# Optimization experiments

Hardware: AMD Instinct MI355X
Metric: run time of the kernel (lower is better)

## Reference

```python
import jax, jax.numpy as jnp
import numpy as np

B, S1, S2, S3, I, O = 4, 64, 64, 64, 32, 32
MX, MZ = 16, 16
HID = O * 2  # factor=2 feedforward hidden


def setup_inputs() -> dict:
    key = jax.random.key(0)
    ks = jax.random.split(key, 5)
    x = jax.random.normal(ks[0], (B, S1, S2, S3, I), jnp.float32)
    # xavier-normal-ish scale for complex fourier weights stored as [...,2]
    sw = np.float32(np.sqrt(2.0 / (I + O)))
    wx = jax.random.normal(ks[1], (I, O, MX, 2), jnp.float32) * sw
    wz = jax.random.normal(ks[2], (I, O, MZ, 2), jnp.float32) * sw
    w1 = jax.random.normal(ks[3], (O, HID), jnp.float32) * np.float32(np.sqrt(1.0 / O))
    b1 = jnp.zeros((HID,), jnp.float32)
    w2 = jax.random.normal(ks[4], (HID, O), jnp.float32) * np.float32(np.sqrt(1.0 / HID))
    b2 = jnp.zeros((O,), jnp.float32)
    return {"x": x, "wx": wx, "wz": wz, "w1": w1, "b1": b1, "w2": w2, "b2": b2}


def _forward_fourier(x, wx, wz):
    # x: [b, i, s1, s2, s3]
    # z-axis branch
    cwz = wz[..., 0] + 1j * wz[..., 1]          # [i, o, mz] complex
    xfz = jnp.fft.rfft(x, axis=-1, norm='ortho')  # [b,i,s1,s2,S3//2+1]
    pz = jnp.einsum('bixyz,ioz->boxyz', xfz[..., :MZ], cwz)
    pz = jnp.pad(pz, ((0, 0), (0, 0), (0, 0), (0, 0), (0, S3 // 2 + 1 - MZ)))
    xz = jnp.fft.irfft(pz, n=S3, axis=-1, norm='ortho')
    # x-axis branch (note: modes_y branch contributes 0 in the source, xy=0.0)
    cwx = wx[..., 0] + 1j * wx[..., 1]          # [i, o, mx]
    xfx = jnp.fft.rfft(x, axis=2, norm='ortho')  # [b,i,S1//2+1,s2,s3]
    px = jnp.einsum('bixyz,iox->boxyz', xfx[:, :, :MX], cwx)
    px = jnp.pad(px, ((0, 0), (0, 0), (0, S1 // 2 + 1 - MX), (0, 0), (0, 0)))
    xx = jnp.fft.irfft(px, n=S1, axis=2, norm='ortho')
    return xx + xz


def reference(x, wx, wz, w1, b1, w2, b2):
    xt = jnp.transpose(x, (0, 4, 1, 2, 3))      # b i s1 s2 s3
    y = _forward_fourier(xt, wx, wz)
    y = jnp.transpose(y, (0, 2, 3, 4, 1))       # b s1 s2 s3 o
    # backcast FeedForward: Linear -> ReLU -> Linear (dropout=0, no norms)
    h = jax.nn.relu(y @ w1 + b1)
    b_out = h @ w2 + b2
    return b_out
```

## Files before the change

### kernel.cpp

```cpp
#include <hip/hip_runtime.h>

namespace {

typedef _Float16 half_t;
typedef half_t f16x8 __attribute__((ext_vector_type(8)));
typedef float f32x4 __attribute__((ext_vector_type(4)));

constexpr size_t RSTR = 64 * 64 * 32;

constexpr int WS_TF = 0;
constexpr int WS_TI = 2048;
constexpr int WS_WZ = 4096;
constexpr int WS_WX = 69632;
constexpr int WS_W1 = 135168;
constexpr int WS_W2 = 137216;

__device__ __forceinline__ float f4get(const float4& v, int u) {
  return u == 0 ? v.x : (u == 1 ? v.y : (u == 2 ? v.z : v.w));
}

__device__ __forceinline__ f32x4 mfma16(f16x8 a, f16x8 b, f32x4 c) {
  return __builtin_amdgcn_mfma_f32_16x16x32_f16(a, b, c, 0, 0, 0);
}

__global__ __launch_bounds__(256) void kinit(const float* __restrict__ wx,
                                             const float* __restrict__ wz,
                                             const float* __restrict__ w1,
                                             const float* __restrict__ w2,
                                             half_t* __restrict__ wsh) {
  const int id = blockIdx.x * 256 + threadIdx.x;
  const int l = id & 63, r = l & 15, g = l >> 4;
  f16x8 frag;
  if (id < 256) {
    int fid = id >> 6, mt = fid >> 1, kt = fid & 1;
#pragma unroll
    for (int e = 0; e < 8; ++e) {
      int k = kt * 32 + 8 * g + e;
      int mc = mt * 16 + r, m = mc >> 1, p = mc & 1;
      float s, c;
      sincospif((float)(m * k) * (1.0f / 32.0f), &s, &c);
      frag[e] = (half_t)(0.125f * (p ? -s : c));
    }
    *(f16x8*)(wsh + WS_TF + (size_t)id * 8) = frag;
  } else if (id < 512) {
    int id2 = id - 256, mt = id2 >> 6;
#pragma unroll
    for (int e = 0; e < 8; ++e) {
      int zp = mt * 16 + r;
      int k = 8 * g + e, m = k >> 1, p = k & 1;
      float s, c;
      sincospif((float)(m * zp) * (1.0f / 32.0f), &s, &c);
      float sc = (m == 0) ? 0.125f : 0.25f;
      frag[e] = (half_t)(p ? -sc * s : sc * c);
    }
    *(f16x8*)(wsh + WS_TI + (size_t)id2 * 8) = frag;
  } else if (id < 16896) {
    int id2 = id - 512;
    const float* wsrc = wz;
    size_t off = WS_WZ;
    if (id2 >= 8192) { id2 -= 8192; wsrc = wx; off = WS_WX; }
    int fid = id2 >> 6, m = fid >> 3, kt = (fid >> 2) & 1, nt = fid & 3;
#pragma unroll
    for (int e = 0; e < 8; ++e) {
      int k = kt * 32 + 8 * g + e, i = k >> 1, p = k & 1;
      int n = nt * 16 + r, o = n >> 1, q = n & 1;
      int base = ((i * 32 + o) * 16 + m) * 2;
      float re = wsrc[base], im = wsrc[base + 1];
      frag[e] = (half_t)(q ? (p ? re : im) : (p ? -im : re));
    }
    *(f16x8*)(wsh + off + (size_t)id2 * 8) = frag;
  } else if (id < 17152) {
    int id2 = id - 16896, nt = id2 >> 6;
#pragma unroll
    for (int e = 0; e < 8; ++e) {
      int k = 8 * g + e, n = nt * 16 + r;
      frag[e] = (half_t)w1[k * 64 + n];
    }
    *(f16x8*)(wsh + WS_W1 + (size_t)id2 * 8) = frag;
  } else if (id < 17408) {
    int id2 = id - 17152, fid = id2 >> 6, kt = fid >> 1, nt = fid & 1;
#pragma unroll
    for (int e = 0; e < 8; ++e) {
      int k = kt * 32 + 8 * g + e, n = nt * 16 + r;
      frag[e] = (half_t)w2[k * 32 + n];
    }
    *(f16x8*)(wsh + WS_W2 + (size_t)id2 * 8) = frag;
  }
}

template <int BR>
__global__ __launch_bounds__(256) void kspec(const float* __restrict__ x,
                                             const half_t* __restrict__ wsh,
                                             const float* __restrict__ b1g,
                                             const float* __restrict__ b2g,
                                             float* __restrict__ outf) {
  __shared__ __align__(16) char smraw[49152];
  half_t* XB = (half_t*)smraw;
  half_t* FB = (half_t*)smraw;
  half_t* PB = (half_t*)(smraw + 32768);
  half_t* YL = (half_t*)smraw;
  half_t* HL = (half_t*)(smraw + 32768);
  half_t* outh = (half_t*)outf;
  const int t = threadIdx.x, l = t & 63, w = t >> 6, r = l & 15, g = l >> 4;
  const f32x4 vzero = {0.f, 0.f, 0.f, 0.f};

  const int col0 = blockIdx.x * 8;
  int b = 0, s2 = 0, s30 = 0;
  size_t xbase, zstr, cstr;
  if (BR == 0) {
    xbase = (size_t)col0 * 2048; zstr = 32; cstr = 2048;
  } else {
    b = col0 >> 12; s2 = (col0 >> 6) & 63; s30 = col0 & 63;
    xbase = (size_t)b * 8388608 + (size_t)s2 * 2048 + (size_t)s30 * 32;
    zstr = RSTR; cstr = 32;
  }

  {
    int c = t >> 5, sub = t & 31;
    int i4 = (sub & 7) * 4, zq = sub >> 3;
    const float* xp = x + xbase + (size_t)c * cstr + i4;
#pragma unroll
    for (int zo = 0; zo < 2; ++zo) {
      int zb = zq * 16 + zo * 8;
      float4 v[8];
#pragma unroll
      for (int zz = 0; zz < 8; ++zz)
        v[zz] = *(const float4*)(xp + (size_t)(zb + zz) * zstr);
#pragma unroll
      for (int u = 0; u < 4; ++u) {
        f16x8 rowv;
#pragma unroll
        for (int zz = 0; zz < 8; ++zz) rowv[zz] = (half_t)f4get(v[zz], u);
        int rowi = c * 32 + i4 + u;
        int gr = (zb >> 3) ^ (rowi & 7);
        *(f16x8*)(XB + rowi * 64 + gr * 8) = rowv;
      }
    }
  }
  __syncthreads();

  f32x4 fa[2][4];
#pragma unroll
  for (int mt = 0; mt < 2; ++mt)
#pragma unroll
    for (int nt = 0; nt < 4; ++nt) fa[mt][nt] = vzero;
  {
    f16x8 Atf[2][2], Bx[4][2];
#pragma unroll
    for (int mt = 0; mt < 2; ++mt)
#pragma unroll
      for (int kt = 0; kt < 2; ++kt)
        Atf[mt][kt] = *(const f16x8*)(wsh + WS_TF + (size_t)((mt * 2 + kt) * 64 + l) * 8);
#pragma unroll
    for (int nt = 0; nt < 4; ++nt)
#pragma unroll
      for (int kt = 0; kt < 2; ++kt) {
        int rowi = w * 64 + nt * 16 + r;
        int gr = (kt * 4 + g) ^ (rowi & 7);
        Bx[nt][kt] = *(const f16x8*)(XB + rowi * 64 + gr * 8);
      }
#pragma unroll
    for (int kt = 0; kt < 2; ++kt)
#pragma unroll
      for (int nt = 0; nt < 4; ++nt)
#pragma unroll
        for (int mt = 0; mt < 2; ++mt)
          fa[mt][nt] = mfma16(Atf[mt][kt], Bx[nt][kt], fa[mt][nt]);
  }
  __syncthreads();

#pragma unroll
  for (int mt = 0; mt < 2; ++mt)
#pragma unroll
    for (int nt = 0; nt < 4; ++nt)
#pragma unroll
      for (int q = 0; q < 4; ++q) {
        int mc = mt * 16 + 4 * g + q, m = mc >> 1, p = mc & 1;
        int n = w * 64 + nt * 16 + r, c = n >> 5, i = n & 31;
        int k = 2 * i + p;
        FB[(m * 16 + c) * 64 + ((k >> 3) ^ (c & 7)) * 8 + (k & 7)] = (half_t)fa[mt][nt][q];
      }
  __syncthreads();

  const half_t* WF = wsh + (BR == 0 ? WS_WZ : WS_WX);
#pragma unroll
  for (int j = 0; j < 4; ++j) {
    int m = w * 4 + j;
    f16x8 Af[2];
#pragma unroll
    for (int kt = 0; kt < 2; ++kt) {
      int gr = (kt * 4 + g) ^ (r & 7);
      Af[kt] = *(const f16x8*)(FB + (m * 16 + r) * 64 + gr * 8);
    }
    f32x4 pa[4];
#pragma unroll
    for (int nt = 0; nt < 4; ++nt) pa[nt] = vzero;
#pragma unroll
    for (int kt = 0; kt < 2; ++kt)
#pragma unroll
      for (int nt = 0; nt < 4; ++nt) {
        f16x8 Bw = *(const f16x8*)(WF + (size_t)((m * 8 + kt * 4 + nt) * 64 + l) * 8);
        pa[nt] = mfma16(Af[kt], Bw, pa[nt]);
      }
#pragma unroll
    for (int nt = 0; nt < 4; ++nt)
#pragma unroll
      for (int q = 0; q < 4; ++q) {
        int c = 4 * g + q;
        if (c < 8) {
          int n = nt * 16 + r, o = n >> 1, q2 = n & 1;
          int k = 2 * m + q2;
          PB[(c * 32 + o) * 32 + ((k >> 3) ^ (o & 3)) * 8 + (k & 7)] = (half_t)pa[nt][q];
        }
      }
  }
  __syncthreads();

  {
    f16x8 Ati[4];
#pragma unroll
    for (int mt = 0; mt < 4; ++mt)
      Ati[mt] = *(const f16x8*)(wsh + WS_TI + (size_t)(mt * 64 + l) * 8);
#pragma unroll
    for (int cc = 0; cc < 2; ++cc) {
      int c = w * 2 + cc;
      f16x8 Bp[2];
#pragma unroll
      for (int nt = 0; nt < 2; ++nt) {
        int o = nt * 16 + r;
        Bp[nt] = *(const f16x8*)(PB + (c * 32 + o) * 32 + (g ^ (o & 3)) * 8);
      }
      f32x4 ya[4][2];
#pragma unroll
      for (int mt = 0; mt < 4; ++mt)
#pragma unroll
        for (int nt = 0; nt < 2; ++nt) ya[mt][nt] = mfma16(Ati[mt], Bp[nt], vzero);
#pragma unroll
      for (int mt = 0; mt < 4; ++mt)
#pragma unroll
        for (int nt = 0; nt < 2; ++nt)
#pragma unroll
          for (int q = 0; q < 4; ++q) {
            int zp = mt * 16 + 4 * g + q, o = nt * 16 + r;
            if (BR == 0) {
              outh[(size_t)(col0 + c) * 4096 + zp * 64 + o] = (half_t)ya[mt][nt][q];
            } else {
              size_t kzcol = (size_t)(b * 64 + zp) * 64 + s2;
              float yz = (float)outh[kzcol * 4096 + (s30 + c) * 64 + o];
              float yv = ya[mt][nt][q] + yz;
              int rowi = c * 64 + zp;
              YL[rowi * 32 + ((o >> 3) ^ (rowi & 3)) * 8 + (o & 7)] = (half_t)yv;
            }
          }
    }
  }
  if (BR == 0) return;
  __syncthreads();

  {
    f16x8 W1F[4], W2F[4];
#pragma unroll
    for (int nt = 0; nt < 4; ++nt)
      W1F[nt] = *(const f16x8*)(wsh + WS_W1 + (size_t)(nt * 64 + l) * 8);
#pragma unroll
    for (int f = 0; f < 4; ++f)
      W2F[f] = *(const f16x8*)(wsh + WS_W2 + (size_t)(f * 64 + l) * 8);
    float b1v[4], b2v[2];
#pragma unroll
    for (int nt = 0; nt < 4; ++nt) b1v[nt] = b1g[nt * 16 + r];
#pragma unroll
    for (int nt = 0; nt < 2; ++nt) b2v[nt] = b2g[nt * 16 + r];

    for (int rr = 0; rr < 4; ++rr) {
      f16x8 AY[2];
#pragma unroll
      for (int mt = 0; mt < 2; ++mt) {
        int rowi = rr * 128 + w * 32 + mt * 16 + r;
        AY[mt] = *(const f16x8*)(YL + rowi * 32 + (g ^ (rowi & 3)) * 8);
      }
      f32x4 ha[2][4];
#pragma unroll
      for (int mt = 0; mt < 2; ++mt)
#pragma unroll
        for (int nt = 0; nt < 4; ++nt) ha[mt][nt] = mfma16(AY[mt], W1F[nt], vzero);
#pragma unroll
      for (int mt = 0; mt < 2; ++mt)
#pragma unroll
        for (int nt = 0; nt < 4; ++nt)
#pragma unroll
          for (int q = 0; q < 4; ++q) {
            int rloc = w * 32 + mt * 16 + 4 * g + q, n = nt * 16 + r;
            float hv = fmaxf(ha[mt][nt][q] + b1v[nt], 0.f);
            HL[rloc * 64 + ((n >> 3) ^ (rloc & 7)) * 8 + (n & 7)] = (half_t)hv;
          }
      __syncthreads();
      f16x8 AH[2][2];
#pragma unroll
      for (int mt = 0; mt < 2; ++mt)
#pragma unroll
        for (int kt = 0; kt < 2; ++kt) {
          int rloc = w * 32 + mt * 16 + r;
          AH[mt][kt] = *(const f16x8*)(HL + rloc * 64 + ((kt * 4 + g) ^ (rloc & 7)) * 8);
        }
      f32x4 oa[2][2];
#pragma unroll
      for (int mt = 0; mt < 2; ++mt)
#pragma unroll
        for (int nt = 0; nt < 2; ++nt) oa[mt][nt] = vzero;
#pragma unroll
      for (int kt = 0; kt < 2; ++kt)
#pragma unroll
        for (int mt = 0; mt < 2; ++mt)
#pragma unroll
          for (int nt = 0; nt < 2; ++nt)
            oa[mt][nt] = mfma16(AH[mt][kt], W2F[kt * 2 + nt], oa[mt][nt]);
#pragma unroll
      for (int mt = 0; mt < 2; ++mt)
#pragma unroll
        for (int nt = 0; nt < 2; ++nt)
#pragma unroll
          for (int q = 0; q < 4; ++q) {
            int rowg = rr * 128 + w * 32 + mt * 16 + 4 * g + q;
            int c = rowg >> 6, zp = rowg & 63, o = nt * 16 + r;
            outf[(size_t)b * 8388608 + (size_t)zp * RSTR + (size_t)s2 * 2048 +
                 (size_t)(s30 + c) * 32 + o] = oa[mt][nt][q] + b2v[nt];
          }
      __syncthreads();
    }
  }
}

}

extern "C" void kernel_launch(void* const* d_in, const int* in_sizes, int n_in,
                              void* d_out, int out_size, void* d_ws, size_t ws_size,
                              hipStream_t stream) {
  const float* x = (const float*)d_in[0];
  const float* wx = (const float*)d_in[1];
  const float* wz = (const float*)d_in[2];
  const float* w1 = (const float*)d_in[3];
  const float* b1 = (const float*)d_in[4];
  const float* w2 = (const float*)d_in[5];
  const float* b2 = (const float*)d_in[6];
  float* out = (float*)d_out;
  half_t* wsh = (half_t*)d_ws;

  hipLaunchKernelGGL(kinit, dim3(68), dim3(256), 0, stream, wx, wz, w1, w2, wsh);
  hipLaunchKernelGGL((kspec<0>), dim3(2048), dim3(256), 0, stream, x, wsh, b1, b2, out);
  hipLaunchKernelGGL((kspec<1>), dim3(2048), dim3(256), 0, stream, x, wsh, b1, b2, out);
}
```

Before: 146.1 us.

## Split x-branch into dedicated smaller-tile kernel with reduced LDS and block swizzle

The x-axis branch plus feedforward moves out of the templated kernel into a new kernel that handles 4 columns per block instead of 8. It uses 32KB of shared memory instead of 48KB and asks for 5 blocks per SM, so more blocks can be resident at once. Block indices are remapped so neighbouring blocks spread across s2/b. The z-branch intermediates are prefetched into registers before the inverse-transform MFMA. The cost is twice as many blocks, each reloading the same weight fragments, and possible register pressure from the launch-bounds hint.

```diff
diff --git a/kernel.cpp b/kernel.cpp
--- a/kernel.cpp
+++ b/kernel.cpp
@@ -98,22 +98,12 @@
   half_t* XB = (half_t*)smraw;
   half_t* FB = (half_t*)smraw;
   half_t* PB = (half_t*)(smraw + 32768);
-  half_t* YL = (half_t*)smraw;
-  half_t* HL = (half_t*)(smraw + 32768);
   half_t* outh = (half_t*)outf;
   const int t = threadIdx.x, l = t & 63, w = t >> 6, r = l & 15, g = l >> 4;
   const f32x4 vzero = {0.f, 0.f, 0.f, 0.f};
 
   const int col0 = blockIdx.x * 8;
-  int b = 0, s2 = 0, s30 = 0;
-  size_t xbase, zstr, cstr;
-  if (BR == 0) {
-    xbase = (size_t)col0 * 2048; zstr = 32; cstr = 2048;
-  } else {
-    b = col0 >> 12; s2 = (col0 >> 6) & 63; s30 = col0 & 63;
-    xbase = (size_t)b * 8388608 + (size_t)s2 * 2048 + (size_t)s30 * 32;
-    zstr = RSTR; cstr = 32;
-  }
+  size_t xbase = (size_t)col0 * 2048, zstr = 32, cstr = 2048;
 
   {
     int c = t >> 5, sub = t & 31;
@@ -182,7 +172,7 @@
       }
   __syncthreads();
 
-  const half_t* WF = wsh + (BR == 0 ? WS_WZ : WS_WX);
+  const half_t* WF = wsh + WS_WZ;
 #pragma unroll
   for (int j = 0; j < 4; ++j) {
     int m = w * 4 + j;
@@ -242,19 +232,163 @@
 #pragma unroll
           for (int q = 0; q < 4; ++q) {
             int zp = mt * 16 + 4 * g + q, o = nt * 16 + r;
-            if (BR == 0) {
-              outh[(size_t)(col0 + c) * 4096 + zp * 64 + o] = (half_t)ya[mt][nt][q];
-            } else {
-              size_t kzcol = (size_t)(b * 64 + zp) * 64 + s2;
-              float yz = (float)outh[kzcol * 4096 + (s30 + c) * 64 + o];
-              float yv = ya[mt][nt][q] + yz;
-              int rowi = c * 64 + zp;
-              YL[rowi * 32 + ((o >> 3) ^ (rowi & 3)) * 8 + (o & 7)] = (half_t)yv;
-            }
+            outh[(size_t)(col0 + c) * 4096 + zp * 64 + o] = (half_t)ya[mt][nt][q];
           }
     }
   }
-  if (BR == 0) return;
+}
+
+__global__ __launch_bounds__(256, 5) void kx4(const float* __restrict__ x,
+                                              const half_t* __restrict__ wsh,
+                                              const float* __restrict__ b1g,
+                                              const float* __restrict__ b2g,
+                                              float* __restrict__ outf) {
+  __shared__ __align__(16) half_t smh[16384];
+  half_t* XB = smh;
+  half_t* FB = smh + 8192;
+  half_t* PB = smh + 12288;
+  half_t* YL = smh;
+  half_t* HL = smh + 8192;
+  half_t* outh = (half_t*)outf;
+  const int t = threadIdx.x, l = t & 63, w = t >> 6, r = l & 15, g = l >> 4;
+  const f32x4 vzero = {0.f, 0.f, 0.f, 0.f};
+
+  const int d = blockIdx.x;
+  const int p = (d & 7) * 512 + (d >> 3);
+  const int col0 = p * 4;
+  const int b = col0 >> 12, s2 = (col0 >> 6) & 63, s30 = col0 & 63;
+  const size_t xbase = (size_t)b * 8388608 + (size_t)s2 * 2048 + (size_t)s30 * 32;
+
+  {
+    int sub = t & 31, zq = t >> 5;
+    int c = sub >> 3, i4 = (sub & 7) * 4;
+    const float* xp = x + xbase + (size_t)c * 32 + i4 + (size_t)(zq * 8) * RSTR;
+    float4 v[8];
+#pragma unroll
+    for (int zz = 0; zz < 8; ++zz) v[zz] = *(const float4*)(xp + (size_t)zz * RSTR);
+#pragma unroll
+    for (int uu = 0; uu < 4; ++uu) {
+      int u = (uu + sub) & 3;
+      f16x8 rowv;
+#pragma unroll
+      for (int zz = 0; zz < 8; ++zz) rowv[zz] = (half_t)f4get(v[zz], u);
+      int rowi = c * 32 + i4 + u;
+      *(f16x8*)(XB + rowi * 64 + (zq ^ (rowi & 7)) * 8) = rowv;
+    }
+  }
+  __syncthreads();
+
+  f32x4 fa[2][2];
+  {
+    f16x8 Atf[2][2], Bx[2][2];
+#pragma unroll
+    for (int mt = 0; mt < 2; ++mt)
+#pragma unroll
+      for (int kt = 0; kt < 2; ++kt)
+        Atf[mt][kt] = *(const f16x8*)(wsh + WS_TF + (size_t)((mt * 2 + kt) * 64 + l) * 8);
+#pragma unroll
+    for (int nt = 0; nt < 2; ++nt)
+#pragma unroll
+      for (int kt = 0; kt < 2; ++kt) {
+        int rowi = w * 32 + nt * 16 + r;
+        Bx[nt][kt] = *(const f16x8*)(XB + rowi * 64 + (((kt * 4 + g) ^ (rowi & 7))) * 8);
+      }
+#pragma unroll
+    for (int mt = 0; mt < 2; ++mt)
+#pragma unroll
+      for (int nt = 0; nt < 2; ++nt) fa[mt][nt] = vzero;
+#pragma unroll
+    for (int kt = 0; kt < 2; ++kt)
+#pragma unroll
+      for (int nt = 0; nt < 2; ++nt)
+#pragma unroll
+        for (int mt = 0; mt < 2; ++mt)
+          fa[mt][nt] = mfma16(Atf[mt][kt], Bx[nt][kt], fa[mt][nt]);
+  }
+#pragma unroll
+  for (int mt = 0; mt < 2; ++mt)
+#pragma unroll
+    for (int nt = 0; nt < 2; ++nt)
+#pragma unroll
+      for (int q = 0; q < 4; ++q) {
+        int mc = mt * 16 + 4 * g + q, m = mc >> 1, pp = mc & 1;
+        int n = w * 32 + nt * 16 + r, c = n >> 5, i = n & 31;
+        int k = 2 * i + pp;
+        FB[(m * 4 + c) * 64 + (((k >> 3) ^ ((m + 2 * c) & 7))) * 8 + (k & 7)] =
+            (half_t)fa[mt][nt][q];
+      }
+  __syncthreads();
+
+#pragma unroll
+  for (int j = 0; j < 4; ++j) {
+    int m = w * 4 + j;
+    int rsel = r & 3, keym = (m + 2 * rsel) & 7;
+    f16x8 Af[2];
+#pragma unroll
+    for (int kt = 0; kt < 2; ++kt)
+      Af[kt] = *(const f16x8*)(FB + (m * 4 + rsel) * 64 + (((kt * 4 + g) ^ keym)) * 8);
+    f32x4 pa[4];
+#pragma unroll
+    for (int nt = 0; nt < 4; ++nt) pa[nt] = vzero;
+#pragma unroll
+    for (int kt = 0; kt < 2; ++kt)
+#pragma unroll
+      for (int nt = 0; nt < 4; ++nt) {
+        f16x8 Bw = *(const f16x8*)(wsh + WS_WX + (size_t)((m * 8 + kt * 4 + nt) * 64 + l) * 8);
+        pa[nt] = mfma16(Af[kt], Bw, pa[nt]);
+      }
+    if (g == 0) {
+#pragma unroll
+      for (int nt = 0; nt < 4; ++nt)
+#pragma unroll
+        for (int q = 0; q < 4; ++q) {
+          int c = q;
+          int n = nt * 16 + r, o = n >> 1, q2 = n & 1;
+          int k = 2 * m + q2;
+          PB[(c * 32 + o) * 32 + (((k >> 3) ^ (o & 3))) * 8 + (k & 7)] = (half_t)pa[nt][q];
+        }
+    }
+  }
+  __syncthreads();
+
+  {
+    half_t yzr[4][2][4];
+    const half_t* yzp = outh + ((size_t)b * 4096 + s2) * 4096 + (size_t)(s30 + w) * 64 +
+                        (size_t)(4 * g) * 262144 + r;
+#pragma unroll
+    for (int mt = 0; mt < 4; ++mt)
+#pragma unroll
+      for (int q = 0; q < 4; ++q)
+#pragma unroll
+        for (int nt = 0; nt < 2; ++nt)
+          yzr[mt][nt][q] = yzp[(size_t)(mt * 16 + q) * 262144 + nt * 16];
+
+    f16x8 Ati[4], Bp[2];
+#pragma unroll
+    for (int mt = 0; mt < 4; ++mt)
+      Ati[mt] = *(const f16x8*)(wsh + WS_TI + (size_t)(mt * 64 + l) * 8);
+#pragma unroll
+    for (int nt = 0; nt < 2; ++nt) {
+      int o = nt * 16 + r;
+      Bp[nt] = *(const f16x8*)(PB + (w * 32 + o) * 32 + ((g ^ (o & 3))) * 8);
+    }
+    f32x4 ya[4][2];
+#pragma unroll
+    for (int mt = 0; mt < 4; ++mt)
+#pragma unroll
+      for (int nt = 0; nt < 2; ++nt) ya[mt][nt] = mfma16(Ati[mt], Bp[nt], vzero);
+#pragma unroll
+    for (int mt = 0; mt < 4; ++mt)
+#pragma unroll
+      for (int nt = 0; nt < 2; ++nt)
+#pragma unroll
+        for (int q = 0; q < 4; ++q) {
+          int zp = mt * 16 + 4 * g + q, o = nt * 16 + r;
+          float acc = ya[mt][nt][q] + (float)yzr[mt][nt][q];
+          int rowi = w * 64 + zp;
+          YL[rowi * 32 + (((o >> 3) ^ ((rowi >> 2) & 3))) * 8 + (o & 7)] = (half_t)acc;
+        }
+  }
   __syncthreads();
 
   {
@@ -272,60 +406,41 @@
     for (int nt = 0; nt < 2; ++nt) b2v[nt] = b2g[nt * 16 + r];
 
     for (int rr = 0; rr < 4; ++rr) {
-      f16x8 AY[2];
-#pragma unroll
-      for (int mt = 0; mt < 2; ++mt) {
-        int rowi = rr * 128 + w * 32 + mt * 16 + r;
-        AY[mt] = *(const f16x8*)(YL + rowi * 32 + (g ^ (rowi & 3)) * 8);
-      }
-      f32x4 ha[2][4];
-#pragma unroll
-      for (int mt = 0; mt < 2; ++mt)
-#pragma unroll
-        for (int nt = 0; nt < 4; ++nt) ha[mt][nt] = mfma16(AY[mt], W1F[nt], vzero);
-#pragma unroll
-      for (int mt = 0; mt < 2; ++mt)
-#pragma unroll
-        for (int nt = 0; nt < 4; ++nt)
-#pragma unroll
-          for (int q = 0; q < 4; ++q) {
-            int rloc = w * 32 + mt * 16 + 4 * g + q, n = nt * 16 + r;
-            float hv = fmaxf(ha[mt][nt][q] + b1v[nt], 0.f);
-            HL[rloc * 64 + ((n >> 3) ^ (rloc & 7)) * 8 + (n & 7)] = (half_t)hv;
-          }
+      int rowA = rr * 64 + w * 16 + r;
+      f16x8 AY = *(const f16x8*)(YL + rowA * 32 + ((g ^ ((rowA >> 2) & 3))) * 8);
+      f32x4 ha[4];
+#pragma unroll
+      for (int nt = 0; nt < 4; ++nt) ha[nt] = mfma16(AY, W1F[nt], vzero);
+#pragma unroll
+      for (int nt = 0; nt < 4; ++nt)
+#pragma unroll
+        for (int q = 0; q < 4; ++q) {
+          int rloc = w * 16 + 4 * g + q, n = nt * 16 + r;
+          float hv = fmaxf(ha[nt][q] + b1v[nt], 0.f);
+          HL[rloc * 64 + (((n >> 3) ^ ((rloc >> 2) & 7))) * 8 + (n & 7)] = (half_t)hv;
+        }
       __syncthreads();
-      f16x8 AH[2][2];
-#pragma unroll
-      for (int mt = 0; mt < 2; ++mt)
-#pragma unroll
-        for (int kt = 0; kt < 2; ++kt) {
-          int rloc = w * 32 + mt * 16 + r;
-          AH[mt][kt] = *(const f16x8*)(HL + rloc * 64 + ((kt * 4 + g) ^ (rloc & 7)) * 8);
+      int rowA2 = w * 16 + r;
+      f16x8 AH[2];
+#pragma unroll
+      for (int kt = 0; kt < 2; ++kt)
+        AH[kt] = *(const f16x8*)(HL + rowA2 * 64 + (((kt * 4 + g) ^ ((rowA2 >> 2) & 7))) * 8);
+      f32x4 oa[2];
+#pragma unroll
+      for (int nt = 0; nt < 2; ++nt) oa[nt] = vzero;
+#pragma unroll
+      for (int kt = 0; kt < 2; ++kt)
+#pragma unroll
+        for (int nt = 0; nt < 2; ++nt) oa[nt] = mfma16(AH[kt], W2F[kt * 2 + nt], oa[nt]);
+#pragma unroll
+      for (int nt = 0; nt < 2; ++nt)
+#pragma unroll
+        for (int q = 0; q < 4; ++q) {
+          int zp2 = w * 16 + 4 * g + q, o = nt * 16 + r;
+          outf[(size_t)b * 8388608 + (size_t)zp2 * RSTR + (size_t)s2 * 2048 +
+               (size_t)(s30 + rr) * 32 + o] = oa[nt][q] + b2v[nt];
         }
-      f32x4 oa[2][2];
-#pragma unroll
-      for (int mt = 0; mt < 2; ++mt)
-#pragma unroll
-        for (int nt = 0; nt < 2; ++nt) oa[mt][nt] = vzero;
-#pragma unroll
-      for (int kt = 0; kt < 2; ++kt)
-#pragma unroll
-        for (int mt = 0; mt < 2; ++mt)
-#pragma unroll
-          for (int nt = 0; nt < 2; ++nt)
-            oa[mt][nt] = mfma16(AH[mt][kt], W2F[kt * 2 + nt], oa[mt][nt]);
-#pragma unroll
-      for (int mt = 0; mt < 2; ++mt)
-#pragma unroll
-        for (int nt = 0; nt < 2; ++nt)
-#pragma unroll
-          for (int q = 0; q < 4; ++q) {
-            int rowg = rr * 128 + w * 32 + mt * 16 + 4 * g + q;
-            int c = rowg >> 6, zp = rowg & 63, o = nt * 16 + r;
-            outf[(size_t)b * 8388608 + (size_t)zp * RSTR + (size_t)s2 * 2048 +
-                 (size_t)(s30 + c) * 32 + o] = oa[mt][nt][q] + b2v[nt];
-          }
-      __syncthreads();
+      if (rr < 3) __syncthreads();
     }
   }
 }
@@ -347,5 +462,5 @@
 
   hipLaunchKernelGGL(kinit, dim3(68), dim3(256), 0, stream, wx, wz, w1, w2, wsh);
   hipLaunchKernelGGL((kspec<0>), dim3(2048), dim3(256), 0, stream, x, wsh, b1, b2, out);
-  hipLaunchKernelGGL((kspec<1>), dim3(2048), dim3(256), 0, stream, x, wsh, b1, b2, out);
-}
+  hipLaunchKernelGGL(kx4, dim3(4096), dim3(256), 0, stream, x, wsh, b1, b2, out);
+}
```

After: 135.5 us. 1.08x faster.
